# Kernel optimization log

Hardware: AMD Instinct MI355X
Metric: run time of the kernel (lower is better)

The kernel has to match this reference:

```python
import jax, jax.numpy as jnp
import numpy as np

N_CLASS = 21
EPS = 1e-07


def setup_inputs() -> dict:
    key = jax.random.key(0)
    k1, k2 = jax.random.split(key)
    shape = (32, 512, 512)
    class_pred = jax.random.randint(k1, shape, 0, N_CLASS, dtype=jnp.int32)
    class_gt = jax.random.randint(k2, shape, 0, N_CLASS, dtype=jnp.int32)
    return {"class_pred": class_pred, "class_gt": class_gt}


def reference(class_pred, class_gt):
    # Single-pass histogram formulation of the original O(n_class) loop.
    pred = class_pred.reshape(-1)
    gt = class_gt.reshape(-1)
    # Per-class counts: bincount with fixed length (jit-compatible).
    pred_counts = jnp.bincount(pred, length=N_CLASS).astype(jnp.float32)
    gt_counts = jnp.bincount(gt, length=N_CLASS).astype(jnp.float32)
    # Intersection per class: count positions where pred == gt == i.
    # Route mismatches to an extra overflow bin (N_CLASS), then drop it.
    match_ids = jnp.where(pred == gt, pred, N_CLASS)
    intersection = jnp.bincount(match_ids, length=N_CLASS + 1)[:N_CLASS].astype(jnp.float32)
    union = pred_counts + gt_counts - intersection
    iou = (intersection + EPS) / (union + EPS)  # [n_class]
    return jnp.mean(iou)
```

## Files before the change

kernel.cpp:

```cpp
#include <hip/hip_runtime.h>

#define NC 21
#define NB (NC * NC)
#define NWAVES 8
#define HPAD 448

__global__ void __launch_bounds__(512) zero_hist(unsigned* __restrict__ h) {
    int i = threadIdx.x;
    if (i < NB) h[i] = 0;
}

__global__ void __launch_bounds__(512) hist_kernel(const int* __restrict__ pred,
                                                   const int* __restrict__ gt,
                                                   unsigned* __restrict__ g_hist,
                                                   int n) {
    __shared__ unsigned h[NWAVES][HPAD];
    const int tid = threadIdx.x;
    const int wave = tid >> 6;

    for (int i = tid; i < NWAVES * HPAD; i += blockDim.x) (&h[0][0])[i] = 0;
    __syncthreads();

    const int n4 = n >> 2;
    const int4* __restrict__ p4 = (const int4*)pred;
    const int4* __restrict__ g4 = (const int4*)gt;
    const int stride = gridDim.x * blockDim.x;
    int gidx = blockIdx.x * blockDim.x + tid;

    for (int i = gidx; i < n4; i += stride) {
        int4 p = p4[i];
        int4 g = g4[i];
        atomicAdd(&h[wave][p.x + NC * g.x], 1u);
        atomicAdd(&h[wave][p.y + NC * g.y], 1u);
        atomicAdd(&h[wave][p.z + NC * g.z], 1u);
        atomicAdd(&h[wave][p.w + NC * g.w], 1u);
    }
    for (int i = (n4 << 2) + gidx; i < n; i += stride) {
        atomicAdd(&h[wave][pred[i] + NC * gt[i]], 1u);
    }
    __syncthreads();

    for (int i = tid; i < NB; i += blockDim.x) {
        unsigned s = 0;
        #pragma unroll
        for (int w = 0; w < NWAVES; ++w) s += h[w][i];
        if (s) atomicAdd(&g_hist[i], s);
    }
}

__global__ void __launch_bounds__(64) miou_final(const unsigned* __restrict__ h,
                                                 float* __restrict__ out) {
    const int lane = threadIdx.x;
    float iou = 0.0f;
    if (lane < NC) {
        float pc = 0.0f, gc = 0.0f;
        #pragma unroll
        for (int g = 0; g < NC; ++g) pc += (float)h[lane + NC * g];
        #pragma unroll
        for (int p = 0; p < NC; ++p) gc += (float)h[p + NC * lane];
        float inter = (float)h[lane * (NC + 1)];
        float uni = pc + gc - inter;
        iou = (inter + 1e-7f) / (uni + 1e-7f);
    }
    for (int off = 32; off; off >>= 1) iou += __shfl_down(iou, off);
    if (lane == 0) out[0] = iou * (1.0f / 21.0f);
}

extern "C" void kernel_launch(void* const* d_in, const int* in_sizes, int n_in,
                              void* d_out, int out_size, void* d_ws, size_t ws_size,
                              hipStream_t stream) {
    const int* pred = (const int*)d_in[0];
    const int* gt   = (const int*)d_in[1];
    unsigned* g_hist = (unsigned*)d_ws;
    float* out = (float*)d_out;
    const int n = in_sizes[0];

    zero_hist<<<1, 512, 0, stream>>>(g_hist);
    hist_kernel<<<512, 512, 0, stream>>>(pred, gt, g_hist, n);
    miou_final<<<1, 64, 0, stream>>>(g_hist, out);
}
```

Baseline: 100.00 us.

## Replace global atomics with per-block partial histograms and a fused reduce kernel

Each block now writes its joint histogram to its own slot in workspace instead of atomically adding into a shared global histogram. This removes the zeroing kernel and the global atomic contention. The final kernel sums all 1024 partials and computes the mIoU. The grid doubles to 1024 blocks, which adds a serial single-block reduction over 1024x441 values that may cost more than the atomics it replaces.

```diff
diff --git a/kernel.cpp b/kernel.cpp
--- a/kernel.cpp
+++ b/kernel.cpp
@@ -4,28 +4,25 @@
 #define NB (NC * NC)
 #define NWAVES 8
 #define HPAD 448
-
-__global__ void __launch_bounds__(512) zero_hist(unsigned* __restrict__ h) {
-    int i = threadIdx.x;
-    if (i < NB) h[i] = 0;
-}
+#define NBLK 1024
 
 __global__ void __launch_bounds__(512) hist_kernel(const int* __restrict__ pred,
                                                    const int* __restrict__ gt,
-                                                   unsigned* __restrict__ g_hist,
+                                                   unsigned* __restrict__ partials,
                                                    int n) {
     __shared__ unsigned h[NWAVES][HPAD];
     const int tid = threadIdx.x;
     const int wave = tid >> 6;
 
-    for (int i = tid; i < NWAVES * HPAD; i += blockDim.x) (&h[0][0])[i] = 0;
+    #pragma unroll
+    for (int i = tid; i < NWAVES * HPAD; i += 512) (&h[0][0])[i] = 0;
     __syncthreads();
 
     const int n4 = n >> 2;
     const int4* __restrict__ p4 = (const int4*)pred;
     const int4* __restrict__ g4 = (const int4*)gt;
-    const int stride = gridDim.x * blockDim.x;
-    int gidx = blockIdx.x * blockDim.x + tid;
+    const int stride = gridDim.x * 512;
+    int gidx = blockIdx.x * 512 + tid;
 
     for (int i = gidx; i < n4; i += stride) {
         int4 p = p4[i];
@@ -40,30 +37,43 @@
     }
     __syncthreads();
 
-    for (int i = tid; i < NB; i += blockDim.x) {
+    unsigned* out = partials + blockIdx.x * NB;
+    for (int i = tid; i < NB; i += 512) {
         unsigned s = 0;
         #pragma unroll
         for (int w = 0; w < NWAVES; ++w) s += h[w][i];
-        if (s) atomicAdd(&g_hist[i], s);
+        out[i] = s;
     }
 }
 
-__global__ void __launch_bounds__(64) miou_final(const unsigned* __restrict__ h,
-                                                 float* __restrict__ out) {
-    const int lane = threadIdx.x;
+__global__ void __launch_bounds__(512) reduce_miou(const unsigned* __restrict__ partials,
+                                                   float* __restrict__ out) {
+    __shared__ unsigned tot[NB];
+    const int tid = threadIdx.x;
+
+    if (tid < NB) {
+        unsigned s = 0;
+        #pragma unroll 8
+        for (int k = 0; k < NBLK; ++k) s += partials[k * NB + tid];
+        tot[tid] = s;
+    }
+    __syncthreads();
+
     float iou = 0.0f;
-    if (lane < NC) {
+    if (tid < NC) {
         float pc = 0.0f, gc = 0.0f;
         #pragma unroll
-        for (int g = 0; g < NC; ++g) pc += (float)h[lane + NC * g];
+        for (int g = 0; g < NC; ++g) pc += (float)tot[tid + NC * g];
         #pragma unroll
-        for (int p = 0; p < NC; ++p) gc += (float)h[p + NC * lane];
-        float inter = (float)h[lane * (NC + 1)];
+        for (int p = 0; p < NC; ++p) gc += (float)tot[p + NC * tid];
+        float inter = (float)tot[tid * (NC + 1)];
         float uni = pc + gc - inter;
         iou = (inter + 1e-7f) / (uni + 1e-7f);
     }
-    for (int off = 32; off; off >>= 1) iou += __shfl_down(iou, off);
-    if (lane == 0) out[0] = iou * (1.0f / 21.0f);
+    if (tid < 64) {
+        for (int off = 32; off; off >>= 1) iou += __shfl_down(iou, off);
+        if (tid == 0) out[0] = iou * (1.0f / 21.0f);
+    }
 }
 
 extern "C" void kernel_launch(void* const* d_in, const int* in_sizes, int n_in,
@@ -71,11 +81,10 @@
                               hipStream_t stream) {
     const int* pred = (const int*)d_in[0];
     const int* gt   = (const int*)d_in[1];
-    unsigned* g_hist = (unsigned*)d_ws;
+    unsigned* partials = (unsigned*)d_ws;
     float* out = (float*)d_out;
     const int n = in_sizes[0];
 
-    zero_hist<<<1, 512, 0, stream>>>(g_hist);
-    hist_kernel<<<512, 512, 0, stream>>>(pred, gt, g_hist, n);
-    miou_final<<<1, 64, 0, stream>>>(g_hist, out);
+    hist_kernel<<<NBLK, 512, 0, stream>>>(pred, gt, partials, n);
+    reduce_miou<<<1, 512, 0, stream>>>(partials, out);
 }
```

Result: slower. 119.4 us (+19.4%).
